# Performance work log

Measured on AMD Instinct MI355X. Metric: run time of the kernel, lower is better.

## Reference

```python
import jax, jax.numpy as jnp
import numpy as np

ALG_DIM = 248      # dim of E8 adjoint rep
NNZ_BASE = 300     # base structure-constant triples (antisymmetrized -> 600 nnz)
N_NODES = 20000
N_EDGES = 160000


def _structure_constants():
    """Deterministic sparse antisymmetric structure constants C_ijk.

    Returns index arrays (ci, cj, ck) int32 and values cv float32 such that
    [x, y]_k = sum_t cv[t] * x[ci[t]] * y[cj[t]] with C antisymmetric in (i, j).
    """
    rng = np.random.default_rng(0)
    i = rng.integers(0, ALG_DIM, NNZ_BASE)
    j = rng.integers(0, ALG_DIM, NNZ_BASE)
    j = np.where(j == i, (j + 1) % ALG_DIM, j)  # bracket of equal basis elts is 0
    k = rng.integers(0, ALG_DIM, NNZ_BASE)
    v = rng.normal(size=NNZ_BASE).astype(np.float32)
    ci = np.concatenate([i, j]).astype(np.int32)
    cj = np.concatenate([j, i]).astype(np.int32)
    ck = np.concatenate([k, k]).astype(np.int32)
    cv = np.concatenate([v, -v]).astype(np.float32)
    return jnp.asarray(ci), jnp.asarray(cj), jnp.asarray(ck), jnp.asarray(cv)


def _bracket(x, y, ci, cj, ck, cv):
    """Sparse Lie bracket [x, y]: x, y have shape (..., ALG_DIM)."""
    terms = x[..., ci] * y[..., cj] * cv          # (..., nnz)
    return jnp.zeros(x.shape, x.dtype).at[..., ck].add(terms)


def setup_inputs() -> dict:
    key = jax.random.key(0)
    k1, k2 = jax.random.split(key)
    features = jax.random.normal(k1, (N_NODES, ALG_DIM), dtype=jnp.float32)
    edge_index = jax.random.randint(k2, (2, N_EDGES), 0, N_NODES, dtype=jnp.int32)
    ci, cj, ck, cv = _structure_constants()
    return {
        "features": features,
        "edge_index": edge_index,
        "ci": ci, "cj": cj, "ck": ck, "cv": cv,
        "alpha_msg": jnp.float32(1.0),     # msg_projection.alpha
        "alpha_bil": jnp.float32(1.0),     # msg_bilinear.alpha
        "alpha_w": jnp.float32(1.0),       # update_W.alpha
        "update_scale": jnp.float32(0.1),
    }


def reference(features, edge_index, ci, cj, ck, cv,
              alpha_msg, alpha_bil, alpha_w, update_scale):
    src_idx = edge_index[0]
    tgt_idx = edge_index[1]
    src = features[src_idx]                        # (E, d) gather
    tgt = features[tgt_idx]                        # (E, d) gather
    # message: alpha_bil * [alpha_msg * src, tgt]
    msg = alpha_bil * _bracket(alpha_msg * src, tgt, ci, cj, ck, cv)
    # scatter-add aggregate into per-node accumulator
    agg = jnp.zeros_like(features).at[tgt_idx].add(msg)
    # bracket-based update: x + agg + scale * [agg, alpha_w * agg]
    upd = _bracket(agg, alpha_w * agg, ci, cj, ck, cv)
    return features + agg + update_scale * upd
```

## Files before the change

kernel.cpp:

```cpp
#include <hip/hip_runtime.h>


#define ALG    248
#define ALG4    62
#define SLOTS   64
#define WPB      4
#define NBLK  1536
#define MAXNNZ 768

struct T8 { int ij; float v; };

__global__ __launch_bounds__(256) void elc_fill(
    const int* __restrict__ ei, int E,
    int* __restrict__ cnt, int* __restrict__ slot,
    const int* __restrict__ ci, const int* __restrict__ cj,
    const int* __restrict__ ck, const float* __restrict__ cv,
    T8* __restrict__ terms, int* __restrict__ koff, int nnz)
{
    const int tid = threadIdx.x;

    if (blockIdx.x == 0) {
        __shared__ int s_cnt[256];
        __shared__ int s_scan[256];
        __shared__ int s_cur[256];
        s_cnt[tid] = 0;
        __syncthreads();
        for (int t = tid; t < nnz; t += 256) atomicAdd(&s_cnt[ck[t]], 1);
        __syncthreads();
        int v = s_cnt[tid];
        s_scan[tid] = v;
        __syncthreads();
        for (int off = 1; off < 256; off <<= 1) {
            int u = (tid >= off) ? s_scan[tid - off] : 0;
            __syncthreads();
            s_scan[tid] += u;
            __syncthreads();
        }
        const int excl = s_scan[tid] - v;
        s_cur[tid] = excl;
        if (tid < ALG) koff[tid] = excl;
        if (tid == 0)  koff[ALG] = nnz;
        __syncthreads();
        for (int t = tid; t < nnz; t += 256) {
            const int p = atomicAdd(&s_cur[ck[t]], 1);
            T8 tm; tm.ij = ci[t] | (cj[t] << 16); tm.v = cv[t];
            terms[p] = tm;
        }
    }

    for (int e = blockIdx.x * 256 + tid; e < E; e += gridDim.x * 256) {
        const int t = ei[E + e];
        const int p = atomicAdd(&cnt[t], 1);
        if (p < SLOTS) slot[t * SLOTS + p] = ei[e];
    }
}

__global__ __launch_bounds__(256) void elc_node(
    const float* __restrict__ feat,
    const int*   __restrict__ cnt,
    const int*   __restrict__ slot,
    const T8*    __restrict__ terms,
    const int*   __restrict__ koff,
    const float* __restrict__ p_am, const float* __restrict__ p_ab,
    const float* __restrict__ p_aw, const float* __restrict__ p_us,
    float* __restrict__ out, int N, int nnz)
{
    __shared__ __align__(8)  T8    s_terms[MAXNNZ];
    __shared__ int s_koff[ALG + 1];
    __shared__ __align__(16) float s_tg[WPB][ALG];
    __shared__ __align__(16) float s_S[WPB][ALG];
    __shared__ float s_ag[WPB][ALG];

    const int tid  = threadIdx.x;
    const int lane = tid & 63;
    const int wave = tid >> 6;
    const float4* feat4 = (const float4*)feat;

    {
        const int2* g = (const int2*)terms;
        int2* s = (int2*)s_terms;
        for (int t = tid; t < nnz; t += 256) s[t] = g[t];
        for (int t = tid; t < ALG + 1; t += 256) s_koff[t] = koff[t];
    }
    __syncthreads();

    int kb[4], ke[4];
#pragma unroll
    for (int q = 0; q < 4; ++q) {
        const int k = lane + 64 * q;
        if (k < ALG) { kb[q] = s_koff[k]; ke[q] = s_koff[k + 1]; }
        else         { kb[q] = 0;         ke[q] = 0; }
    }

    const float cab   = (*p_ab) * (*p_am);
    const float scale = (*p_us) * (*p_aw);

    float* tg = s_tg[wave];
    float* S  = s_S[wave];
    float* ag = s_ag[wave];

    const int stride = NBLK * WPB;
    int n = blockIdx.x * WPB + wave;

    int deg_c = 0, sn_c = 0;
    float4 tgt_c = make_float4(0.f, 0.f, 0.f, 0.f);
    if (n < N) {
        deg_c = min(cnt[n], SLOTS);
        sn_c  = slot[n * SLOTS + lane];
        if (lane < ALG4) tgt_c = feat4[(size_t)n * ALG4 + lane];
    }

    int    nP   = -1;
    float4 accP = make_float4(0.f, 0.f, 0.f, 0.f);
    float4 tgtP = make_float4(0.f, 0.f, 0.f, 0.f);

    while (n < N) {
        const int n_next = n + stride;

        float4 f[8];
#pragma unroll
        for (int d = 0; d < 8; ++d) {
            f[d] = make_float4(0.f, 0.f, 0.f, 0.f);
            const int sd = __shfl(sn_c, d);
            if (d < deg_c && lane < ALG4)
                f[d] = feat4[(size_t)sd * ALG4 + lane];
        }

        int deg_n = 0, sn_n = 0;
        float4 tgt_n = make_float4(0.f, 0.f, 0.f, 0.f);
        if (n_next < N) {
            deg_n = min(cnt[n_next], SLOTS);
            sn_n  = slot[n_next * SLOTS + lane];
            if (lane < ALG4) tgt_n = feat4[(size_t)n_next * ALG4 + lane];
        }

        if (nP >= 0) {
            if (lane < ALG4) {
                ((float4*)tg)[lane] = tgtP;
                ((float4*)S)[lane]  = accP;
            }
            float aggk[4] = {0.f, 0.f, 0.f, 0.f};
#pragma unroll
            for (int q = 0; q < 4; ++q)
                for (int t = kb[q]; t < ke[q]; ++t) {
                    const T8 c = s_terms[t];
                    const int i = c.ij & 0xffff;
                    const int j = ((unsigned)c.ij) >> 16;
                    aggk[q] += c.v * S[i] * tg[j];
                }
#pragma unroll
            for (int q = 0; q < 4; ++q) {
                const int k = lane + 64 * q;
                if (k < ALG) { aggk[q] *= cab; ag[k] = aggk[q]; }
            }
            float updk[4] = {0.f, 0.f, 0.f, 0.f};
#pragma unroll
            for (int q = 0; q < 4; ++q)
                for (int t = kb[q]; t < ke[q]; ++t) {
                    const T8 c = s_terms[t];
                    const int i = c.ij & 0xffff;
                    const int j = ((unsigned)c.ij) >> 16;
                    updk[q] += c.v * ag[i] * ag[j];
                }
#pragma unroll
            for (int q = 0; q < 4; ++q) {
                const int k = lane + 64 * q;
                if (k < ALG)
                    out[(size_t)nP * ALG + k] = tg[k] + aggk[q] + scale * updk[q];
            }
        }

        float4 acc = make_float4(0.f, 0.f, 0.f, 0.f);
#pragma unroll
        for (int d = 0; d < 8; ++d) {
            acc.x += f[d].x; acc.y += f[d].y;
            acc.z += f[d].z; acc.w += f[d].w;
        }
        for (int d = 8; d < deg_c; ++d) {
            const int sd = __shfl(sn_c, d);
            if (lane < ALG4) {
                const float4 fd = feat4[(size_t)sd * ALG4 + lane];
                acc.x += fd.x; acc.y += fd.y; acc.z += fd.z; acc.w += fd.w;
            }
        }

        nP = n; accP = acc; tgtP = tgt_c;
        n = n_next; deg_c = deg_n; sn_c = sn_n; tgt_c = tgt_n;
    }

    if (nP >= 0) {
        if (lane < ALG4) {
            ((float4*)tg)[lane] = tgtP;
            ((float4*)S)[lane]  = accP;
        }
        float aggk[4] = {0.f, 0.f, 0.f, 0.f};
#pragma unroll
        for (int q = 0; q < 4; ++q)
            for (int t = kb[q]; t < ke[q]; ++t) {
                const T8 c = s_terms[t];
                const int i = c.ij & 0xffff;
                const int j = ((unsigned)c.ij) >> 16;
                aggk[q] += c.v * S[i] * tg[j];
            }
#pragma unroll
        for (int q = 0; q < 4; ++q) {
            const int k = lane + 64 * q;
            if (k < ALG) { aggk[q] *= cab; ag[k] = aggk[q]; }
        }
        float updk[4] = {0.f, 0.f, 0.f, 0.f};
#pragma unroll
        for (int q = 0; q < 4; ++q)
            for (int t = kb[q]; t < ke[q]; ++t) {
                const T8 c = s_terms[t];
                const int i = c.ij & 0xffff;
                const int j = ((unsigned)c.ij) >> 16;
                updk[q] += c.v * ag[i] * ag[j];
            }
#pragma unroll
        for (int q = 0; q < 4; ++q) {
            const int k = lane + 64 * q;
            if (k < ALG)
                out[(size_t)nP * ALG + k] = tg[k] + aggk[q] + scale * updk[q];
        }
    }
}

extern "C" void kernel_launch(void* const* d_in, const int* in_sizes, int n_in,
                              void* d_out, int out_size, void* d_ws, size_t ws_size,
                              hipStream_t stream) {
    const float* feat = (const float*)d_in[0];
    const int*   ei   = (const int*)d_in[1];
    const int*   ci   = (const int*)d_in[2];
    const int*   cj   = (const int*)d_in[3];
    const int*   ck   = (const int*)d_in[4];
    const float* cv   = (const float*)d_in[5];
    const float* p_am = (const float*)d_in[6];
    const float* p_ab = (const float*)d_in[7];
    const float* p_aw = (const float*)d_in[8];
    const float* p_us = (const float*)d_in[9];
    float* out = (float*)d_out;

    const int N   = in_sizes[0] / ALG;
    const int E   = in_sizes[1] / 2;
    const int nnz = in_sizes[5];

    char* w = (char*)d_ws;
    T8*  terms = (T8*)w;                  w += (size_t)MAXNNZ * sizeof(T8);
    int* koff  = (int*)w;                 w += (size_t)(ALG + 4) * sizeof(int);
    int* cnt   = (int*)w;                 w += (size_t)N * sizeof(int);
    int* slot  = (int*)w;

    hipMemsetAsync(cnt, 0, (size_t)N * sizeof(int), stream);

    elc_fill<<<640, 256, 0, stream>>>(ei, E, cnt, slot,
                                      ci, cj, ck, cv, terms, koff, nnz);
    elc_node<<<NBLK, 256, 0, stream>>>(feat, cnt, slot, terms, koff,
                                       p_am, p_ab, p_aw, p_us, out, N, nnz);
}
```

Before: 159.0 us.

## Distribute bracket terms evenly across lanes in registers with segmented LDS atomics

Before, each lane owned up to four output components k and walked a variable-length term list, so the lane with the most terms set the pace and terms were reread from shared memory. Now the sorted structure-constant terms are padded to 640 and striped 10 per lane into registers. Each lane accumulates runs that share the same k and flushes them with shared-memory atomicAdd, which balances work across lanes at the cost of LDS atomics and an extra zeroing pass. The block and grid counts are also raised, and i/j are packed into 8-bit fields, which assumes nnz ≤ 640 and dimension ≤ 256.

```diff
diff --git a/kernel.cpp b/kernel.cpp
--- a/kernel.cpp
+++ b/kernel.cpp
@@ -5,25 +5,29 @@
 #define ALG4    62
 #define SLOTS   64
 #define WPB      4
-#define NBLK  1536
-#define MAXNNZ 768
-
-struct T8 { int ij; float v; };
+#define NBLK  2048
+#define TPL     10
+#define NPAD   640
 
 __global__ __launch_bounds__(256) void elc_fill(
     const int* __restrict__ ei, int E,
     int* __restrict__ cnt, int* __restrict__ slot,
     const int* __restrict__ ci, const int* __restrict__ cj,
     const int* __restrict__ ck, const float* __restrict__ cv,
-    T8* __restrict__ terms, int* __restrict__ koff, int nnz)
+    int* __restrict__ g_tij, float* __restrict__ g_tv, int nnz)
 {
     const int tid = threadIdx.x;
 
     if (blockIdx.x == 0) {
-        __shared__ int s_cnt[256];
-        __shared__ int s_scan[256];
-        __shared__ int s_cur[256];
+        __shared__ int   s_cnt[256];
+        __shared__ int   s_scan[256];
+        __shared__ int   s_cur[256];
+        __shared__ int   ls_k[NPAD];
+        __shared__ int   ls_ij[NPAD];
+        __shared__ float ls_v[NPAD];
+
         s_cnt[tid] = 0;
+        for (int t = tid; t < NPAD; t += 256) { ls_k[t] = 0; ls_ij[t] = 0; ls_v[t] = 0.f; }
         __syncthreads();
         for (int t = tid; t < nnz; t += 256) atomicAdd(&s_cnt[ck[t]], 1);
         __syncthreads();
@@ -36,15 +40,23 @@
             s_scan[tid] += u;
             __syncthreads();
         }
-        const int excl = s_scan[tid] - v;
-        s_cur[tid] = excl;
-        if (tid < ALG) koff[tid] = excl;
-        if (tid == 0)  koff[ALG] = nnz;
+        s_cur[tid] = s_scan[tid] - v;
         __syncthreads();
         for (int t = tid; t < nnz; t += 256) {
-            const int p = atomicAdd(&s_cur[ck[t]], 1);
-            T8 tm; tm.ij = ci[t] | (cj[t] << 16); tm.v = cv[t];
-            terms[p] = tm;
+            const int k = ck[t];
+            const int p = atomicAdd(&s_cur[k], 1);
+            ls_k[p]  = k;
+            ls_ij[p] = ci[t] | (cj[t] << 8);
+            ls_v[p]  = cv[t];
+        }
+        __syncthreads();
+        for (int p = tid; p < NPAD; p += 256) {
+            const int k  = ls_k[p];
+            const int fl = (p + 1 < NPAD && ls_k[p + 1] == k) ? 0 : 1;
+            const int w  = ls_ij[p] | (k << 16) | (fl << 24);
+            const int phys = (p % TPL) * 64 + (p / TPL);
+            g_tij[phys] = w;
+            g_tv[phys]  = ls_v[p];
         }
     }
 
@@ -59,14 +71,12 @@
     const float* __restrict__ feat,
     const int*   __restrict__ cnt,
     const int*   __restrict__ slot,
-    const T8*    __restrict__ terms,
-    const int*   __restrict__ koff,
+    const int*   __restrict__ g_tij,
+    const float* __restrict__ g_tv,
     const float* __restrict__ p_am, const float* __restrict__ p_ab,
     const float* __restrict__ p_aw, const float* __restrict__ p_us,
-    float* __restrict__ out, int N, int nnz)
+    float* __restrict__ out, int N)
 {
-    __shared__ __align__(8)  T8    s_terms[MAXNNZ];
-    __shared__ int s_koff[ALG + 1];
     __shared__ __align__(16) float s_tg[WPB][ALG];
     __shared__ __align__(16) float s_S[WPB][ALG];
     __shared__ float s_ag[WPB][ALG];
@@ -76,20 +86,12 @@
     const int wave = tid >> 6;
     const float4* feat4 = (const float4*)feat;
 
-    {
-        const int2* g = (const int2*)terms;
-        int2* s = (int2*)s_terms;
-        for (int t = tid; t < nnz; t += 256) s[t] = g[t];
-        for (int t = tid; t < ALG + 1; t += 256) s_koff[t] = koff[t];
-    }
-    __syncthreads();
-
-    int kb[4], ke[4];
-#pragma unroll
-    for (int q = 0; q < 4; ++q) {
-        const int k = lane + 64 * q;
-        if (k < ALG) { kb[q] = s_koff[k]; ke[q] = s_koff[k + 1]; }
-        else         { kb[q] = 0;         ke[q] = 0; }
+    int   tw[TPL];
+    float tv[TPL];
+#pragma unroll
+    for (int d = 0; d < TPL; ++d) {
+        tw[d] = g_tij[d * 64 + lane];
+        tv[d] = g_tv[d * 64 + lane];
     }
 
     const float cab   = (*p_ab) * (*p_am);
@@ -114,21 +116,24 @@
     float4 accP = make_float4(0.f, 0.f, 0.f, 0.f);
     float4 tgtP = make_float4(0.f, 0.f, 0.f, 0.f);
 
-    while (n < N) {
-        const int n_next = n + stride;
+    while (true) {
+        const bool have_cur = (n < N);
+        const int  n_next   = n + stride;
 
         float4 f[8];
-#pragma unroll
-        for (int d = 0; d < 8; ++d) {
-            f[d] = make_float4(0.f, 0.f, 0.f, 0.f);
-            const int sd = __shfl(sn_c, d);
-            if (d < deg_c && lane < ALG4)
-                f[d] = feat4[(size_t)sd * ALG4 + lane];
+        if (have_cur) {
+#pragma unroll
+            for (int d = 0; d < 8; ++d) {
+                f[d] = make_float4(0.f, 0.f, 0.f, 0.f);
+                const int sd = __shfl(sn_c, d);
+                if (d < deg_c && lane < ALG4)
+                    f[d] = feat4[(size_t)sd * ALG4 + lane];
+            }
         }
 
         int deg_n = 0, sn_n = 0;
         float4 tgt_n = make_float4(0.f, 0.f, 0.f, 0.f);
-        if (n_next < N) {
+        if (have_cur && n_next < N) {
             deg_n = min(cnt[n_next], SLOTS);
             sn_n  = slot[n_next * SLOTS + lane];
             if (lane < ALG4) tgt_n = feat4[(size_t)n_next * ALG4 + lane];
@@ -139,36 +144,49 @@
                 ((float4*)tg)[lane] = tgtP;
                 ((float4*)S)[lane]  = accP;
             }
-            float aggk[4] = {0.f, 0.f, 0.f, 0.f};
-#pragma unroll
-            for (int q = 0; q < 4; ++q)
-                for (int t = kb[q]; t < ke[q]; ++t) {
-                    const T8 c = s_terms[t];
-                    const int i = c.ij & 0xffff;
-                    const int j = ((unsigned)c.ij) >> 16;
-                    aggk[q] += c.v * S[i] * tg[j];
-                }
 #pragma unroll
             for (int q = 0; q < 4; ++q) {
                 const int k = lane + 64 * q;
-                if (k < ALG) { aggk[q] *= cab; ag[k] = aggk[q]; }
-            }
-            float updk[4] = {0.f, 0.f, 0.f, 0.f};
-#pragma unroll
-            for (int q = 0; q < 4; ++q)
-                for (int t = kb[q]; t < ke[q]; ++t) {
-                    const T8 c = s_terms[t];
-                    const int i = c.ij & 0xffff;
-                    const int j = ((unsigned)c.ij) >> 16;
-                    updk[q] += c.v * ag[i] * ag[j];
+                if (k < ALG) ag[k] = 0.f;
+            }
+            float acc = 0.f;
+#pragma unroll
+            for (int d = 0; d < TPL; ++d) {
+                const int w = tw[d];
+                const int i = w & 255;
+                const int j = (w >> 8) & 255;
+                acc = fmaf(tv[d] * S[i], tg[j], acc);
+                if ((w & (1 << 24)) || d == TPL - 1) {
+                    atomicAdd(&ag[(w >> 16) & 255], cab * acc);
+                    acc = 0.f;
                 }
+            }
+#pragma unroll
+            for (int q = 0; q < 4; ++q) {
+                const int k = lane + 64 * q;
+                if (k < ALG) S[k] = tg[k] + ag[k];
+            }
+            float acc2 = 0.f;
+#pragma unroll
+            for (int d = 0; d < TPL; ++d) {
+                const int w = tw[d];
+                const int i = w & 255;
+                const int j = (w >> 8) & 255;
+                acc2 = fmaf(tv[d] * ag[i], ag[j], acc2);
+                if ((w & (1 << 24)) || d == TPL - 1) {
+                    atomicAdd(&S[(w >> 16) & 255], scale * acc2);
+                    acc2 = 0.f;
+                }
+            }
 #pragma unroll
             for (int q = 0; q < 4; ++q) {
                 const int k = lane + 64 * q;
                 if (k < ALG)
-                    out[(size_t)nP * ALG + k] = tg[k] + aggk[q] + scale * updk[q];
-            }
-        }
+                    out[(size_t)nP * ALG + k] = S[k];
+            }
+        }
+
+        if (!have_cur) break;
 
         float4 acc = make_float4(0.f, 0.f, 0.f, 0.f);
 #pragma unroll
@@ -186,42 +204,6 @@
 
         nP = n; accP = acc; tgtP = tgt_c;
         n = n_next; deg_c = deg_n; sn_c = sn_n; tgt_c = tgt_n;
-    }
-
-    if (nP >= 0) {
-        if (lane < ALG4) {
-            ((float4*)tg)[lane] = tgtP;
-            ((float4*)S)[lane]  = accP;
-        }
-        float aggk[4] = {0.f, 0.f, 0.f, 0.f};
-#pragma unroll
-        for (int q = 0; q < 4; ++q)
-            for (int t = kb[q]; t < ke[q]; ++t) {
-                const T8 c = s_terms[t];
-                const int i = c.ij & 0xffff;
-                const int j = ((unsigned)c.ij) >> 16;
-                aggk[q] += c.v * S[i] * tg[j];
-            }
-#pragma unroll
-        for (int q = 0; q < 4; ++q) {
-            const int k = lane + 64 * q;
-            if (k < ALG) { aggk[q] *= cab; ag[k] = aggk[q]; }
-        }
-        float updk[4] = {0.f, 0.f, 0.f, 0.f};
-#pragma unroll
-        for (int q = 0; q < 4; ++q)
-            for (int t = kb[q]; t < ke[q]; ++t) {
-                const T8 c = s_terms[t];
-                const int i = c.ij & 0xffff;
-                const int j = ((unsigned)c.ij) >> 16;
-                updk[q] += c.v * ag[i] * ag[j];
-            }
-#pragma unroll
-        for (int q = 0; q < 4; ++q) {
-            const int k = lane + 64 * q;
-            if (k < ALG)
-                out[(size_t)nP * ALG + k] = tg[k] + aggk[q] + scale * updk[q];
-        }
     }
 }
 
@@ -245,15 +227,15 @@
     const int nnz = in_sizes[5];
 
     char* w = (char*)d_ws;
-    T8*  terms = (T8*)w;                  w += (size_t)MAXNNZ * sizeof(T8);
-    int* koff  = (int*)w;                 w += (size_t)(ALG + 4) * sizeof(int);
-    int* cnt   = (int*)w;                 w += (size_t)N * sizeof(int);
-    int* slot  = (int*)w;
+    int*   g_tij = (int*)w;               w += (size_t)NPAD * sizeof(int);
+    float* g_tv  = (float*)w;             w += (size_t)NPAD * sizeof(float);
+    int*   cnt   = (int*)w;               w += (size_t)N * sizeof(int);
+    int*   slot  = (int*)w;
 
     hipMemsetAsync(cnt, 0, (size_t)N * sizeof(int), stream);
 
-    elc_fill<<<640, 256, 0, stream>>>(ei, E, cnt, slot,
-                                      ci, cj, ck, cv, terms, koff, nnz);
-    elc_node<<<NBLK, 256, 0, stream>>>(feat, cnt, slot, terms, koff,
-                                       p_am, p_ab, p_aw, p_us, out, N, nnz);
+    elc_fill<<<1024, 256, 0, stream>>>(ei, E, cnt, slot,
+                                       ci, cj, ck, cv, g_tij, g_tv, nnz);
+    elc_node<<<NBLK, 256, 0, stream>>>(feat, cnt, slot, g_tij, g_tv,
+                                       p_am, p_ab, p_aw, p_us, out, N);
 }
```

After: 162.4 us. +2.2%, slower.
